# Optimization experiments

Measured on AMD Instinct MI355X. Metric: run time of the kernel, lower is better.

## Reference

```python
import jax, jax.numpy as jnp
import numpy as np

D_MODEL = 4096
D_FIBER = 16
D_CONTROL = 64
EMA_MOMENTUM = 0.9


def setup_inputs() -> dict:
    key = jax.random.key(0)
    k_h, k_f, k_w1, k_w2 = jax.random.split(key, 4)
    B, S = 4, 2048
    hidden = jax.random.normal(k_h, (B, S, D_MODEL), dtype=jnp.float32)
    # torch nn.Linear stores weight as [out, in]; fiber_proj init: normal std=0.02
    W_fiber = jax.random.normal(k_f, (D_FIBER, D_MODEL), dtype=jnp.float32) * 0.02
    # predictor[0]: Linear(d_model+d_fiber, d_control) with default torch init (uniform)
    fan_in1 = D_MODEL + D_FIBER
    bound1 = 1.0 / np.sqrt(fan_in1)
    W1 = jax.random.uniform(k_w1, (D_CONTROL, fan_in1), dtype=jnp.float32, minval=-bound1, maxval=bound1)
    b1 = jnp.zeros((D_CONTROL,), dtype=jnp.float32)
    # predictor[-2]: Linear(d_control, 1), weight normal std=0.01, bias zero
    W2 = jax.random.normal(k_w2, (1, D_CONTROL), dtype=jnp.float32) * 0.01
    b2 = jnp.zeros((1,), dtype=jnp.float32)
    lam = jnp.asarray(1.0, dtype=jnp.float32)
    return {"hidden": hidden, "W_fiber": W_fiber, "W1": W1, "b1": b1, "W2": W2, "b2": b2, "lam": lam}


def _causal_ema(delta_h, alpha):
    # h_t = alpha*h_{t-1} + (1-alpha)*d_t, h_{-1} = 0. delta_h: [B,S]
    B = delta_h.shape[0]
    def step(h_prev, d_t):
        h_t = alpha * h_prev + (1.0 - alpha) * d_t
        return h_t, h_t
    _, hs = jax.lax.scan(step, jnp.zeros((B,), delta_h.dtype), jnp.swapaxes(delta_h, 0, 1))
    return jnp.swapaxes(hs, 0, 1)  # [B,S]


def reference(hidden, W_fiber, W1, b1, W2, b2, lam):
    h = hidden.astype(jnp.float32)                      # [B,S,D]
    fiber = jnp.einsum('bsd,fd->bsf', h, W_fiber)       # [B,S,16]
    combined = jnp.concatenate([h, fiber], axis=-1)     # [B,S,D+16]
    z = jax.nn.gelu(jnp.einsum('bsc,kc->bsk', combined, W1) + b1, approximate=False)
    delta_h = jax.nn.softplus(jnp.einsum('bsk,ok->bso', z, W2) + b2)[..., 0]  # [B,S]
    field = _causal_ema(delta_h, EMA_MOMENTUM)          # [B,S]
    gate = jax.nn.sigmoid(-lam * field)
    return gate.astype(hidden.dtype), field.astype(hidden.dtype), delta_h.mean()
```

## Files before the change

### kernel.cpp

```cpp
#include <hip/hip_runtime.h>
#include <hip/hip_bf16.h>

#define D_MODEL 4096
#define NTOK    8192
#define SEQ     2048

typedef short bf16x8 __attribute__((ext_vector_type(8)));
typedef float f32x4  __attribute__((ext_vector_type(4)));

__device__ __forceinline__ short f2bf(float x) {
  __hip_bfloat16 h = __float2bfloat16(x);
  return *reinterpret_cast<short*>(&h);
}
__device__ __forceinline__ float bfs2f(unsigned short u) {
  unsigned int x = ((unsigned int)u) << 16;
  float f;
  __builtin_memcpy(&f, &x, 4);
  return f;
}
__device__ __forceinline__ float bf2f(const void* p, size_t i) {
  return bfs2f(((const unsigned short*)p)[i]);
}

__device__ __forceinline__ void gload_lds16(const void* g, void* l) {
  __builtin_amdgcn_global_load_lds(
      (__attribute__((address_space(1))) void*)(g),
      (__attribute__((address_space(3))) void*)(l), 16, 0, 0);
}

__device__ __forceinline__ int sniff_wave(const unsigned short* p, int n) {
  int lane = threadIdx.x & 63;
  int S = n / 2 < 64 ? n / 2 : 64;
  bool act = lane < S;
  unsigned short ve = 0, vo = 0;
  if (act) { ve = p[2 * lane]; vo = p[2 * lane + 1]; }
  int ee = (ve >> 7) & 0xFF, eo = (vo >> 7) & 0xFF;
  bool ve_band   = (ve == 0) || (ve == 0x8000) || (ee >= 96 && ee <= 141);
  bool vo_bandnz = (vo != 0) && (vo != 0x8000) && (eo >= 96 && eo <= 141);
  int zp = __popcll(__ballot(act && ve == 0 && vo == 0));
  int ob = __popcll(__ballot(act && ve == 0 && vo_bandnz));
  int eb = __popcll(__ballot(act && ve_band));
  if (zp == S) return 1;
  if (4 * ob >= 3 * S) return 0;
  if (4 * eb >= 3 * S) return 1;
  return 0;
}

__device__ __forceinline__ float decode_lam(const void* lamp) {
  unsigned short l0 = *(const unsigned short*)lamp;
  int le = (l0 >> 7) & 0xFF;
  if (l0 != 0 && l0 != 0x8000 && le >= 96 && le <= 141)
    return bfs2f(l0);
  return *(const float*)lamp;
}
__device__ __forceinline__ float decode_b2(const void* p) {
  unsigned short c0 = *(const unsigned short*)p;
  int ce = (c0 >> 7) & 0xFF;
  if (c0 == 0) return 0.0f;
  if (c0 != 0x8000 && ce >= 96 && ce <= 141)
    return bfs2f(c0);
  return *(const float*)p;
}

__global__ __launch_bounds__(256) void fold_w1(const void* __restrict__ W1v,
                                               const void* __restrict__ Wfv,
                                               short* __restrict__ W1eff) {
  int n = blockIdx.x;
  int fw1 = sniff_wave((const unsigned short*)W1v, 64 * 4112);
  int fwf = sniff_wave((const unsigned short*)Wfv, 16 * D_MODEL);
  __shared__ float w1b[16];
  if (threadIdx.x < 16) {
    size_t idx = (size_t)n * 4112 + 4096 + threadIdx.x;
    w1b[threadIdx.x] = fw1 ? bf2f(W1v, idx) : ((const float*)W1v)[idx];
  }
  __syncthreads();
  for (int it = 0; it < 4; ++it) {
    int k0 = it * 1024 + threadIdx.x * 4;
    size_t idx = (size_t)n * 4112 + k0;
    float v0, v1, v2, v3;
    if (fw1) {
      ushort4 u = *(const ushort4*)((const unsigned short*)W1v + idx);
      v0 = bfs2f(u.x); v1 = bfs2f(u.y); v2 = bfs2f(u.z); v3 = bfs2f(u.w);
    } else {
      float4 f = *(const float4*)((const float*)W1v + idx);
      v0 = f.x; v1 = f.y; v2 = f.z; v3 = f.w;
    }
#pragma unroll
    for (int f = 0; f < 16; ++f) {
      size_t wi = (size_t)f * D_MODEL + k0;
      float w0, w1_, w2_, w3_;
      if (fwf) {
        ushort4 u = *(const ushort4*)((const unsigned short*)Wfv + wi);
        w0 = bfs2f(u.x); w1_ = bfs2f(u.y); w2_ = bfs2f(u.z); w3_ = bfs2f(u.w);
      } else {
        float4 fv = *(const float4*)((const float*)Wfv + wi);
        w0 = fv.x; w1_ = fv.y; w2_ = fv.z; w3_ = fv.w;
      }
      float s = w1b[f];
      v0 += s * w0; v1 += s * w1_; v2 += s * w2_; v3 += s * w3_;
    }
    ushort4 o;
    o.x = (unsigned short)f2bf(v0); o.y = (unsigned short)f2bf(v1);
    o.z = (unsigned short)f2bf(v2); o.w = (unsigned short)f2bf(v3);
    *(ushort4*)(W1eff + (size_t)n * D_MODEL + k0) = o;
  }
}

__global__ __launch_bounds__(512, 4) void gemm_part(const void* __restrict__ hid,
                                                    const short* __restrict__ B_,
                                                    float* __restrict__ part) {
  int c = blockIdx.x >> 6;
  int t = blockIdx.x & 63;
  int w    = threadIdx.x >> 6;
  int lane = threadIdx.x & 63;
  int m = lane & 15, kg = lane >> 4;

  __shared__ short Bs[64 * 512];

  int fhid = sniff_wave((const unsigned short*)hid, NTOK * D_MODEL);

#pragma unroll
  for (int i = 0; i < 8; ++i) {
    int n = w * 8 + i;
    const char* src = (const char*)(B_ + (size_t)n * D_MODEL + c * 512) +
                      ((lane ^ (n & 7)) * 16);
    gload_lds16(src, (char*)Bs + n * 1024);
  }

  f32x4 acc0 = {0.f, 0.f, 0.f, 0.f};
  f32x4 acc1 = acc0, acc2 = acc0, acc3 = acc0;
  size_t abase = (size_t)(t * 128 + w * 16 + m) * D_MODEL + c * 512 + kg * 8;

  if (fhid) {
    const short* Ap = (const short*)hid + abase;
    bf16x8 areg[16];
#pragma unroll
    for (int i = 0; i < 16; ++i) areg[i] = *(const bf16x8*)(Ap + i * 32);
    __syncthreads();
#pragma unroll
    for (int s = 0; s < 16; ++s) {
      int u  = s * 4 + kg;
      int sw = (u ^ (m & 7)) * 16;
      bf16x8 b0 = *(const bf16x8*)((const char*)Bs + (m +  0) * 1024 + sw);
      bf16x8 b1 = *(const bf16x8*)((const char*)Bs + (m + 16) * 1024 + sw);
      bf16x8 b2 = *(const bf16x8*)((const char*)Bs + (m + 32) * 1024 + sw);
      bf16x8 b3 = *(const bf16x8*)((const char*)Bs + (m + 48) * 1024 + sw);
      acc0 = __builtin_amdgcn_mfma_f32_16x16x32_bf16(areg[s], b0, acc0, 0, 0, 0);
      acc1 = __builtin_amdgcn_mfma_f32_16x16x32_bf16(areg[s], b1, acc1, 0, 0, 0);
      acc2 = __builtin_amdgcn_mfma_f32_16x16x32_bf16(areg[s], b2, acc2, 0, 0, 0);
      acc3 = __builtin_amdgcn_mfma_f32_16x16x32_bf16(areg[s], b3, acc3, 0, 0, 0);
    }
  } else {
    const float* Ap = (const float*)hid + abase;
    __syncthreads();
    for (int s = 0; s < 16; ++s) {
      float4 lo = *(const float4*)(Ap + s * 32);
      float4 hi = *(const float4*)(Ap + s * 32 + 4);
      bf16x8 a;
      a[0] = f2bf(lo.x); a[1] = f2bf(lo.y); a[2] = f2bf(lo.z); a[3] = f2bf(lo.w);
      a[4] = f2bf(hi.x); a[5] = f2bf(hi.y); a[6] = f2bf(hi.z); a[7] = f2bf(hi.w);
      int u  = s * 4 + kg;
      int sw = (u ^ (m & 7)) * 16;
      bf16x8 b0 = *(const bf16x8*)((const char*)Bs + (m +  0) * 1024 + sw);
      bf16x8 b1 = *(const bf16x8*)((const char*)Bs + (m + 16) * 1024 + sw);
      bf16x8 b2 = *(const bf16x8*)((const char*)Bs + (m + 32) * 1024 + sw);
      bf16x8 b3 = *(const bf16x8*)((const char*)Bs + (m + 48) * 1024 + sw);
      acc0 = __builtin_amdgcn_mfma_f32_16x16x32_bf16(a, b0, acc0, 0, 0, 0);
      acc1 = __builtin_amdgcn_mfma_f32_16x16x32_bf16(a, b1, acc1, 0, 0, 0);
      acc2 = __builtin_amdgcn_mfma_f32_16x16x32_bf16(a, b2, acc2, 0, 0, 0);
      acc3 = __builtin_amdgcn_mfma_f32_16x16x32_bf16(a, b3, acc3, 0, 0, 0);
    }
  }

  float* po = part + ((size_t)c * NTOK + (size_t)t * 128 + w * 16) * 64;
#pragma unroll
  for (int r = 0; r < 4; ++r) {
    int row = kg * 4 + r;
    po[row * 64 + (m +  0)] = acc0[r];
    po[row * 64 + (m + 16)] = acc1[r];
    po[row * 64 + (m + 32)] = acc2[r];
    po[row * 64 + (m + 48)] = acc3[r];
  }
}

__global__ __launch_bounds__(256) void delta_ep(const float* __restrict__ part,
                                                const void* __restrict__ b1,
                                                const void* __restrict__ w2,
                                                const void* __restrict__ b2p,
                                                float* __restrict__ delta) {
  int t   = blockIdx.x & 63;
  int sub = blockIdx.x >> 6;
  int tok = t * 128 + sub * 16 + (threadIdx.x >> 4);
  int cid = threadIdx.x & 15;
  int fb1 = sniff_wave((const unsigned short*)b1, 64);
  int fw2 = sniff_wave((const unsigned short*)w2, 64);
  float y = 0.f;
#pragma unroll
  for (int j = 0; j < 4; ++j) {
    int col = cid + 16 * j;
    float s = 0.f;
#pragma unroll
    for (int c = 0; c < 8; ++c)
      s += part[((size_t)c * NTOK + tok) * 64 + col];
    s += fb1 ? bf2f(b1, col) : ((const float*)b1)[col];
    float g = 0.5f * s * (1.0f + erff(s * 0.70710678118654752f));
    y += g * (fw2 ? bf2f(w2, col) : ((const float*)w2)[col]);
  }
#pragma unroll
  for (int off = 1; off <= 8; off <<= 1) y += __shfl_xor(y, off, 64);
  if (cid == 0) {
    float x = y + decode_b2(b2p);
    float d = (x > 20.0f) ? x : log1pf(expf(x));
    delta[tok] = d;
  }
}

__global__ __launch_bounds__(256) void ema_out(const float* __restrict__ delta,
                                               const void* __restrict__ lamp,
                                               float* __restrict__ out) {
  int b    = threadIdx.x >> 6;
  int lane = threadIdx.x & 63;
  const float alpha = 0.9f;
  float d[32];
  const float* dp = delta + b * SEQ + lane * 32;
  float beta = 0.f, lsum = 0.f;
#pragma unroll
  for (int i = 0; i < 32; ++i) {
    d[i] = dp[i];
    lsum += d[i];
    beta = alpha * beta + 0.1f * d[i];
  }
  float accA = 0.03433683820292512f;
  float accB = beta;
  for (int off = 1; off < 64; off <<= 1) {
    float uA = __shfl_up(accA, off, 64);
    float uB = __shfl_up(accB, off, 64);
    if (lane >= off) {
      accB = accB + accA * uB;
      accA = accA * uA;
    }
  }
  float prev = __shfl_up(accB, 1, 64);
  float h = (lane == 0) ? 0.f : prev;
  float lam = decode_lam(lamp);
#pragma unroll
  for (int i = 0; i < 32; ++i) {
    h = alpha * h + 0.1f * d[i];
    float gate = 1.0f / (1.0f + expf(lam * h));
    out[b * SEQ + lane * 32 + i]        = gate;
    out[NTOK + b * SEQ + lane * 32 + i] = h;
  }
#pragma unroll
  for (int off = 32; off >= 1; off >>= 1) lsum += __shfl_xor(lsum, off, 64);
  __shared__ float bs[4];
  if (lane == 0) bs[b] = lsum;
  __syncthreads();
  if (threadIdx.x == 0)
    out[2 * NTOK] = (bs[0] + bs[1] + bs[2] + bs[3]) * (1.0f / 8192.0f);
}

extern "C" void kernel_launch(void* const* d_in, const int* in_sizes, int n_in,
                              void* d_out, int out_size, void* d_ws, size_t ws_size,
                              hipStream_t stream) {
  const void* hidden = d_in[0];
  const void* Wf     = d_in[1];
  const void* W1     = d_in[2];
  const void* b1     = d_in[3];
  const void* W2     = d_in[4];
  const void* b2     = d_in[5];
  const void* lam    = d_in[6];
  float* out = (float*)d_out;

  char* ws = (char*)d_ws;
  short* W1eff = (short*)ws;
  float* delta = (float*)(ws + (size_t)64 * D_MODEL * 2);
  float* part  = (float*)(ws + (size_t)64 * D_MODEL * 2 + NTOK * 4);

  fold_w1<<<64, 256, 0, stream>>>(W1, Wf, W1eff);
  gemm_part<<<512, 512, 0, stream>>>(hidden, W1eff, part);
  delta_ep<<<512, 256, 0, stream>>>(part, b1, W2, b2, delta);
  ema_out<<<1, 256, 0, stream>>>(delta, lam, out);
}
```

Before: 230.8 us.

## Stage hidden tile in LDS via direct loads, read folded weights from global

The GEMM now uses 64-token tiles with 256 threads. The hidden activations go through LDS using swizzled global-to-LDS loads, and the small folded W1 operand is read straight from global memory, where it should stay cache resident. Block indexing becomes token-major so the 8 K-chunks of a tile are adjacent, which may improve L2 locality, and the epilogue token indexing is simplified to match. The new path relies on a per-wave vmcnt wait with no block barrier, since each wave reads only the LDS rows it loaded. The per-iteration global B loads could add latency, and the grid doubles.

```diff
diff --git a/kernel.cpp b/kernel.cpp
--- a/kernel.cpp
+++ b/kernel.cpp
@@ -106,65 +106,62 @@
   }
 }
 
-__global__ __launch_bounds__(512, 4) void gemm_part(const void* __restrict__ hid,
+__global__ __launch_bounds__(256, 2) void gemm_part(const void* __restrict__ hid,
                                                     const short* __restrict__ B_,
                                                     float* __restrict__ part) {
-  int c = blockIdx.x >> 6;
-  int t = blockIdx.x & 63;
+  int t = blockIdx.x >> 3;
+  int c = blockIdx.x & 7;
   int w    = threadIdx.x >> 6;
   int lane = threadIdx.x & 63;
   int m = lane & 15, kg = lane >> 4;
 
-  __shared__ short Bs[64 * 512];
+  __shared__ short As[64 * 512];
 
   int fhid = sniff_wave((const unsigned short*)hid, NTOK * D_MODEL);
-
-#pragma unroll
-  for (int i = 0; i < 8; ++i) {
-    int n = w * 8 + i;
-    const char* src = (const char*)(B_ + (size_t)n * D_MODEL + c * 512) +
-                      ((lane ^ (n & 7)) * 16);
-    gload_lds16(src, (char*)Bs + n * 1024);
-  }
 
   f32x4 acc0 = {0.f, 0.f, 0.f, 0.f};
   f32x4 acc1 = acc0, acc2 = acc0, acc3 = acc0;
-  size_t abase = (size_t)(t * 128 + w * 16 + m) * D_MODEL + c * 512 + kg * 8;
+
+  const short* Bp = B_ + (size_t)m * D_MODEL + c * 512 + kg * 8;
 
   if (fhid) {
-    const short* Ap = (const short*)hid + abase;
-    bf16x8 areg[16];
-#pragma unroll
-    for (int i = 0; i < 16; ++i) areg[i] = *(const bf16x8*)(Ap + i * 32);
-    __syncthreads();
+#pragma unroll
+    for (int i = 0; i < 16; ++i) {
+      int n = w * 16 + i;
+      const char* src = (const char*)hid +
+          ((size_t)(t * 64 + n) * D_MODEL + c * 512) * 2 +
+          ((lane ^ (n & 7)) * 16);
+      gload_lds16(src, (char*)As + n * 1024);
+    }
+    asm volatile("s_waitcnt vmcnt(0)" ::: "memory");
 #pragma unroll
     for (int s = 0; s < 16; ++s) {
       int u  = s * 4 + kg;
-      int sw = (u ^ (m & 7)) * 16;
-      bf16x8 b0 = *(const bf16x8*)((const char*)Bs + (m +  0) * 1024 + sw);
-      bf16x8 b1 = *(const bf16x8*)((const char*)Bs + (m + 16) * 1024 + sw);
-      bf16x8 b2 = *(const bf16x8*)((const char*)Bs + (m + 32) * 1024 + sw);
-      bf16x8 b3 = *(const bf16x8*)((const char*)Bs + (m + 48) * 1024 + sw);
-      acc0 = __builtin_amdgcn_mfma_f32_16x16x32_bf16(areg[s], b0, acc0, 0, 0, 0);
-      acc1 = __builtin_amdgcn_mfma_f32_16x16x32_bf16(areg[s], b1, acc1, 0, 0, 0);
-      acc2 = __builtin_amdgcn_mfma_f32_16x16x32_bf16(areg[s], b2, acc2, 0, 0, 0);
-      acc3 = __builtin_amdgcn_mfma_f32_16x16x32_bf16(areg[s], b3, acc3, 0, 0, 0);
+      int row = w * 16 + m;
+      bf16x8 a = *(const bf16x8*)((const char*)As + row * 1024 +
+                                  ((u ^ (m & 7)) * 16));
+      bf16x8 b0 = *(const bf16x8*)(Bp + (size_t)0 * 16 * D_MODEL + s * 32);
+      bf16x8 b1 = *(const bf16x8*)(Bp + (size_t)1 * 16 * D_MODEL + s * 32);
+      bf16x8 b2 = *(const bf16x8*)(Bp + (size_t)2 * 16 * D_MODEL + s * 32);
+      bf16x8 b3 = *(const bf16x8*)(Bp + (size_t)3 * 16 * D_MODEL + s * 32);
+      acc0 = __builtin_amdgcn_mfma_f32_16x16x32_bf16(a, b0, acc0, 0, 0, 0);
+      acc1 = __builtin_amdgcn_mfma_f32_16x16x32_bf16(a, b1, acc1, 0, 0, 0);
+      acc2 = __builtin_amdgcn_mfma_f32_16x16x32_bf16(a, b2, acc2, 0, 0, 0);
+      acc3 = __builtin_amdgcn_mfma_f32_16x16x32_bf16(a, b3, acc3, 0, 0, 0);
     }
   } else {
-    const float* Ap = (const float*)hid + abase;
-    __syncthreads();
+    const float* Ap = (const float*)hid +
+        (size_t)(t * 64 + w * 16 + m) * D_MODEL + c * 512 + kg * 8;
     for (int s = 0; s < 16; ++s) {
       float4 lo = *(const float4*)(Ap + s * 32);
       float4 hi = *(const float4*)(Ap + s * 32 + 4);
       bf16x8 a;
       a[0] = f2bf(lo.x); a[1] = f2bf(lo.y); a[2] = f2bf(lo.z); a[3] = f2bf(lo.w);
       a[4] = f2bf(hi.x); a[5] = f2bf(hi.y); a[6] = f2bf(hi.z); a[7] = f2bf(hi.w);
-      int u  = s * 4 + kg;
-      int sw = (u ^ (m & 7)) * 16;
-      bf16x8 b0 = *(const bf16x8*)((const char*)Bs + (m +  0) * 1024 + sw);
-      bf16x8 b1 = *(const bf16x8*)((const char*)Bs + (m + 16) * 1024 + sw);
-      bf16x8 b2 = *(const bf16x8*)((const char*)Bs + (m + 32) * 1024 + sw);
-      bf16x8 b3 = *(const bf16x8*)((const char*)Bs + (m + 48) * 1024 + sw);
+      bf16x8 b0 = *(const bf16x8*)(Bp + (size_t)0 * 16 * D_MODEL + s * 32);
+      bf16x8 b1 = *(const bf16x8*)(Bp + (size_t)1 * 16 * D_MODEL + s * 32);
+      bf16x8 b2 = *(const bf16x8*)(Bp + (size_t)2 * 16 * D_MODEL + s * 32);
+      bf16x8 b3 = *(const bf16x8*)(Bp + (size_t)3 * 16 * D_MODEL + s * 32);
       acc0 = __builtin_amdgcn_mfma_f32_16x16x32_bf16(a, b0, acc0, 0, 0, 0);
       acc1 = __builtin_amdgcn_mfma_f32_16x16x32_bf16(a, b1, acc1, 0, 0, 0);
       acc2 = __builtin_amdgcn_mfma_f32_16x16x32_bf16(a, b2, acc2, 0, 0, 0);
@@ -172,7 +169,7 @@
     }
   }
 
-  float* po = part + ((size_t)c * NTOK + (size_t)t * 128 + w * 16) * 64;
+  float* po = part + ((size_t)c * NTOK + (size_t)t * 64 + w * 16) * 64;
 #pragma unroll
   for (int r = 0; r < 4; ++r) {
     int row = kg * 4 + r;
@@ -188,9 +185,7 @@
                                                 const void* __restrict__ w2,
                                                 const void* __restrict__ b2p,
                                                 float* __restrict__ delta) {
-  int t   = blockIdx.x & 63;
-  int sub = blockIdx.x >> 6;
-  int tok = t * 128 + sub * 16 + (threadIdx.x >> 4);
+  int tok = blockIdx.x * 16 + (threadIdx.x >> 4);
   int cid = threadIdx.x & 15;
   int fb1 = sniff_wave((const unsigned short*)b1, 64);
   int fw2 = sniff_wave((const unsigned short*)w2, 64);
@@ -277,7 +272,7 @@
   float* part  = (float*)(ws + (size_t)64 * D_MODEL * 2 + NTOK * 4);
 
   fold_w1<<<64, 256, 0, stream>>>(W1, Wf, W1eff);
-  gemm_part<<<512, 512, 0, stream>>>(hidden, W1eff, part);
+  gemm_part<<<1024, 256, 0, stream>>>(hidden, W1eff, part);
   delta_ep<<<512, 256, 0, stream>>>(part, b1, W2, b2, delta);
   ema_out<<<1, 256, 0, stream>>>(delta, lam, out);
 }
```

After: 227.2 us. About the same (-1.5%).
